# Performance work log

Measured on AMD Instinct MI355X. Metric: run time of the kernel, lower is better.

Reference implementation:

```python
import jax, jax.numpy as jnp
import numpy as np

N_NODES = 100000
N_EDGES = 3200000
F_IN = 256
D_OUT = 64
BATCH = 4096
N_FIELDS = 20


def setup_inputs() -> dict:
    key = jax.random.key(0)
    k1, k2, k3, k4 = jax.random.split(key, 4)
    features = jax.random.normal(k1, (N_NODES, F_IN), dtype=jnp.float32)
    edge_index = jax.random.randint(k2, (2, N_EDGES), 0, N_NODES, dtype=jnp.int32)
    W = jax.random.normal(k3, (F_IN, D_OUT), dtype=jnp.float32) * 0.05
    b = jnp.zeros((D_OUT,), dtype=jnp.float32)
    x = jax.random.randint(k4, (BATCH, N_FIELDS), 0, N_NODES, dtype=jnp.int32)
    return {"features": features, "edge_index": edge_index, "W": W, "b": b, "x": x}


def reference(features, edge_index, W, b, x):
    # PyG GCNConv: add self-loops, symmetric normalization, linear transform,
    # scatter-add aggregation, then final index by x.
    n = features.shape[0]
    loop = jnp.arange(n, dtype=edge_index.dtype)
    src = jnp.concatenate([edge_index[0], loop])  # [E+N]
    dst = jnp.concatenate([edge_index[1], loop])
    ones = jnp.ones(src.shape[0], dtype=features.dtype)
    deg = jax.ops.segment_sum(ones, dst, num_segments=n)  # in-degree incl. self-loop
    deg_inv_sqrt = jnp.where(deg > 0, jax.lax.rsqrt(deg), 0.0)
    norm = deg_inv_sqrt[src] * deg_inv_sqrt[dst]  # [E+N]
    xw = features @ W  # [N, D] -- transform before aggregation (fewer FLOPs)
    msg = xw[src] * norm[:, None]  # gather + scale
    out = jax.ops.segment_sum(msg, dst, num_segments=n) + b  # [N, D]
    return out[x]  # [batch, num_fields, D]
```

## Files before the change

kernel.cpp:

```cpp
#include <hip/hip_runtime.h>
#include <hip/hip_bf16.h>

#define N_NODES 100000
#define N_EDGES 3200000
#define F_IN 256
#define D_OUT 64
#define BATCH 4096
#define N_FIELDS 20
#define N_ENTRIES (BATCH * N_FIELDS)

#define NBUCKET 512
#define NPB 196
#define N_PAD (NBUCKET * NPB)
#define EPB 8192
#define NBLK ((N_EDGES + EPB - 1) / EPB)
#define BUCKET_CAP 8192
#define SCAN_B 512
#define NSB (N_PAD / SCAN_B)

typedef short bf16x8 __attribute__((ext_vector_type(8)));
typedef float f32x4 __attribute__((ext_vector_type(4)));

static __device__ __forceinline__ float bfbits2f(unsigned short u) {
    return __uint_as_float((unsigned)u << 16);
}
static __device__ __forceinline__ unsigned short f2bf_bits(float x) {
    __hip_bfloat16 h = __float2bfloat16(x);
    return *reinterpret_cast<unsigned short*>(&h);
}

__global__ __launch_bounds__(256) void k_hist(const uint4* __restrict__ dst4,
                                              unsigned short* __restrict__ perBlockCnt) {
    __shared__ unsigned hist[NBUCKET];
    hist[threadIdx.x] = 0;
    hist[threadIdx.x + 256] = 0;
    __syncthreads();
    int base4 = blockIdx.x * (EPB / 4);
#pragma unroll
    for (int k = 0; k < EPB / 1024; k++) {
        int e4 = base4 + k * 256 + threadIdx.x;
        if (e4 < N_EDGES / 4) {
            uint4 d = dst4[e4];
            atomicAdd(&hist[d.x / NPB], 1u);
            atomicAdd(&hist[d.y / NPB], 1u);
            atomicAdd(&hist[d.z / NPB], 1u);
            atomicAdd(&hist[d.w / NPB], 1u);
        }
    }
    __syncthreads();
    perBlockCnt[(threadIdx.x) * NBLK + blockIdx.x] = (unsigned short)hist[threadIdx.x];
    perBlockCnt[(threadIdx.x + 256) * NBLK + blockIdx.x] = (unsigned short)hist[threadIdx.x + 256];
}

__global__ __launch_bounds__(256) void k_colscan_w(unsigned short* __restrict__ perBlockCnt,
                                                   int* __restrict__ bucketTot) {
    int gw = (blockIdx.x * 256 + threadIdx.x) >> 6;
    int lane = threadIdx.x & 63;
    if (gw >= NBUCKET) return;
    unsigned running = 0;
    for (int c = 0; c < (NBLK + 63) / 64; c++) {
        int blk = c * 64 + lane;
        int idx = gw * NBLK + blk;
        unsigned v = (blk < NBLK) ? perBlockCnt[idx] : 0;
        unsigned orig = v;
#pragma unroll
        for (int d = 1; d < 64; d <<= 1) {
            unsigned t = __shfl_up(v, d, 64);
            if (lane >= d) v += t;
        }
        if (blk < NBLK) perBlockCnt[idx] = (unsigned short)(running + v - orig);
        running += __shfl(v, 63, 64);
    }
    if (lane == 0) bucketTot[gw] = (int)running;
}

__global__ __launch_bounds__(512) void k_basescan(const int* __restrict__ bucketTot,
                                                  int* __restrict__ bucketBase) {
    __shared__ int sh[NBUCKET];
    int tid = threadIdx.x;
    int v = bucketTot[tid];
    sh[tid] = v;
    __syncthreads();
    for (int off = 1; off < NBUCKET; off <<= 1) {
        int t = (tid >= off) ? sh[tid - off] : 0;
        __syncthreads();
        sh[tid] += t;
        __syncthreads();
    }
    bucketBase[tid] = sh[tid] - v;
    if (tid == NBUCKET - 1) bucketBase[NBUCKET] = sh[NBUCKET - 1];
}

__global__ __launch_bounds__(256) void k_bucket_scatter(const uint4* __restrict__ src4,
                                                        const uint4* __restrict__ dst4,
                                                        const int* __restrict__ bucketBase,
                                                        const unsigned short* __restrict__ perBlockCnt,
                                                        unsigned* __restrict__ bucketData) {
    __shared__ unsigned slotBase[NBUCKET];
    slotBase[threadIdx.x] = (unsigned)bucketBase[threadIdx.x] +
                            (unsigned)perBlockCnt[threadIdx.x * NBLK + blockIdx.x];
    slotBase[threadIdx.x + 256] = (unsigned)bucketBase[threadIdx.x + 256] +
                                  (unsigned)perBlockCnt[(threadIdx.x + 256) * NBLK + blockIdx.x];
    __syncthreads();
    int base4 = blockIdx.x * (EPB / 4);
#pragma unroll
    for (int k = 0; k < EPB / 1024; k++) {
        int e4 = base4 + k * 256 + threadIdx.x;
        if (e4 < N_EDGES / 4) {
            uint4 s = src4[e4];
            uint4 d = dst4[e4];
            unsigned ss[4] = {s.x, s.y, s.z, s.w};
            unsigned dd[4] = {d.x, d.y, d.z, d.w};
#pragma unroll
            for (int j = 0; j < 4; j++) {
                unsigned b = dd[j] / NPB;
                unsigned ld = dd[j] - b * NPB;
                unsigned slot = atomicAdd(&slotBase[b], 1u);
                bucketData[slot] = ss[j] | (ld << 17);
            }
        }
    }
}

__global__ __launch_bounds__(256) void kx_cnt(const int* __restrict__ x,
                                              int* __restrict__ nodeEntCnt,
                                              unsigned* __restrict__ refBits) {
    int ent = blockIdx.x * blockDim.x + threadIdx.x;
    if (ent < N_ENTRIES) {
        int node = x[ent];
        atomicAdd(&nodeEntCnt[node], 1);
        atomicOr(&refBits[node >> 5], 1u << (node & 31));
    }
}

__global__ __launch_bounds__(512) void kx_scan_local(const int* __restrict__ nodeEntCnt,
                                                     int* __restrict__ localE,
                                                     int* __restrict__ blockSumsE) {
    __shared__ int sh[SCAN_B];
    int g = blockIdx.x * SCAN_B + threadIdx.x;
    int v = (g < N_PAD) ? nodeEntCnt[g] : 0;
    sh[threadIdx.x] = v;
    __syncthreads();
    for (int off = 1; off < SCAN_B; off <<= 1) {
        int t = (threadIdx.x >= off) ? sh[threadIdx.x - off] : 0;
        __syncthreads();
        sh[threadIdx.x] += t;
        __syncthreads();
    }
    int incl = sh[threadIdx.x];
    if (g < N_PAD) localE[g] = incl - v;
    if (threadIdx.x == SCAN_B - 1) blockSumsE[blockIdx.x] = incl;
}

__global__ __launch_bounds__(256) void kx_scan_blocks(const int* __restrict__ blockSumsE,
                                                      int* __restrict__ blockBaseE) {
    __shared__ int sh[256];
    int tid = threadIdx.x;
    int v = (tid < NSB) ? blockSumsE[tid] : 0;
    sh[tid] = v;
    __syncthreads();
    for (int off = 1; off < 256; off <<= 1) {
        int t = (tid >= off) ? sh[tid - off] : 0;
        __syncthreads();
        sh[tid] += t;
        __syncthreads();
    }
    if (tid < NSB) blockBaseE[tid] = sh[tid] - v;
}

__global__ __launch_bounds__(256) void kx_scatter(const int* __restrict__ x,
                                                  int* __restrict__ localE,
                                                  const int* __restrict__ blockBaseE,
                                                  int* __restrict__ entGrouped) {
    int ent = blockIdx.x * blockDim.x + threadIdx.x;
    if (ent < N_ENTRIES) {
        int node = x[ent];
        int posL = atomicAdd(&localE[node], 1);
        entGrouped[blockBaseE[node >> 9] + posL] = ent;
    }
}

__global__ __launch_bounds__(256) void k_bucket_csr(unsigned* __restrict__ bucketData,
                                                    const int* __restrict__ bucketBase,
                                                    const unsigned* __restrict__ refBits,
                                                    int* __restrict__ rowStart,
                                                    unsigned short* __restrict__ deg) {
    __shared__ unsigned words[BUCKET_CAP];
    __shared__ unsigned srcsorted[BUCKET_CAP];
    __shared__ unsigned nodeCount[NPB];
    __shared__ unsigned sscan[256];
    __shared__ unsigned cursor[NPB];
    __shared__ unsigned char refF[NPB];

    int b = blockIdx.x;
    int base = bucketBase[b];
    int cnt = bucketBase[b + 1] - base;
    if (cnt > BUCKET_CAP) cnt = BUCKET_CAP;
    int tid = threadIdx.x;

    for (int j = tid; j < NPB; j += 256) nodeCount[j] = 0;
    __syncthreads();

    for (int i = tid; i < cnt; i += 256) {
        unsigned w = bucketData[base + i];
        words[i] = w;
        atomicAdd(&nodeCount[w >> 17], 1u);
    }
    __syncthreads();

    int firstNode = b * NPB;
    unsigned refCnt = 0;
    if (tid < NPB) {
        int node = firstNode + tid;
        unsigned isRef = (refBits[node >> 5] >> (node & 31)) & 1u;
        refF[tid] = (unsigned char)isRef;
        refCnt = isRef ? nodeCount[tid] : 0;
        deg[node] = (unsigned short)nodeCount[tid];
    }
    sscan[tid] = refCnt;
    __syncthreads();
    for (int off = 1; off < 256; off <<= 1) {
        unsigned t = (tid >= off) ? sscan[tid - off] : 0;
        __syncthreads();
        sscan[tid] += t;
        __syncthreads();
    }

    if (tid < NPB) {
        unsigned excl = sscan[tid] - refCnt;
        rowStart[firstNode + tid] = base + (int)excl;
        cursor[tid] = excl;
    }
    __syncthreads();

    for (int i = tid; i < cnt; i += 256) {
        unsigned w = words[i];
        unsigned ld = w >> 17;
        if (refF[ld]) {
            unsigned slot = atomicAdd(&cursor[ld], 1u);
            srcsorted[slot] = w & 0x1FFFFu;
        }
    }
    __syncthreads();

    int refTotal = (int)sscan[255];
    for (int i = tid; i < refTotal; i += 256)
        bucketData[base + i] = srcsorted[i];
}

__global__ void k_wtconv(const float* __restrict__ W, unsigned short* __restrict__ WTbf) {
    int i = blockIdx.x * blockDim.x + threadIdx.x;
    if (i >= D_OUT * F_IN) return;
    int n = i >> 8, k = i & 255;
    WTbf[i] = f2bf_bits(W[k * D_OUT + n]);
}

__global__ __launch_bounds__(256) void k_gemm_mfma(const float* __restrict__ feat,
                                                   const unsigned short* __restrict__ WTbf,
                                                   const unsigned short* __restrict__ deg,
                                                   unsigned short* __restrict__ y) {
    __shared__ unsigned short wt[64 * 264];
    int tid = threadIdx.x;
    {
        int r = tid >> 2, seg = tid & 3;
        const uint4* gsrc = (const uint4*)(WTbf + r * 256 + seg * 64);
        uint4* ldst = (uint4*)&wt[r * 264 + seg * 64];
#pragma unroll
        for (int q = 0; q < 8; q++) ldst[q] = gsrc[q];
    }
    __syncthreads();

    int wave = tid >> 6, lane = tid & 63;
    int quad = lane >> 4, m = lane & 15;
    int rowT = blockIdx.x * 64 + wave * 16;
    int row = rowT + m;
    int rowC = (row < N_NODES) ? row : (N_NODES - 1);
    const float* fb = feat + (size_t)rowC * F_IN + quad * 8;

    f32x4 acc0 = {0.f, 0.f, 0.f, 0.f};
    f32x4 acc1 = acc0, acc2 = acc0, acc3 = acc0;

#pragma unroll
    for (int kk = 0; kk < 8; kk++) {
        float4 x0 = *(const float4*)(fb + kk * 32);
        float4 x1 = *(const float4*)(fb + kk * 32 + 4);
        bf16x8 a;
        a[0] = (short)f2bf_bits(x0.x); a[1] = (short)f2bf_bits(x0.y);
        a[2] = (short)f2bf_bits(x0.z); a[3] = (short)f2bf_bits(x0.w);
        a[4] = (short)f2bf_bits(x1.x); a[5] = (short)f2bf_bits(x1.y);
        a[6] = (short)f2bf_bits(x1.z); a[7] = (short)f2bf_bits(x1.w);
        int kbase = kk * 32 + quad * 8;
        bf16x8 b0 = *(const bf16x8*)&wt[(0 * 16 + m) * 264 + kbase];
        bf16x8 b1 = *(const bf16x8*)&wt[(1 * 16 + m) * 264 + kbase];
        bf16x8 b2 = *(const bf16x8*)&wt[(2 * 16 + m) * 264 + kbase];
        bf16x8 b3 = *(const bf16x8*)&wt[(3 * 16 + m) * 264 + kbase];
        acc0 = __builtin_amdgcn_mfma_f32_16x16x32_bf16(a, b0, acc0, 0, 0, 0);
        acc1 = __builtin_amdgcn_mfma_f32_16x16x32_bf16(a, b1, acc1, 0, 0, 0);
        acc2 = __builtin_amdgcn_mfma_f32_16x16x32_bf16(a, b2, acc2, 0, 0, 0);
        acc3 = __builtin_amdgcn_mfma_f32_16x16x32_bf16(a, b3, acc3, 0, 0, 0);
    }

    float dv[4];
#pragma unroll
    for (int r = 0; r < 4; r++) {
        int rr = rowT + quad * 4 + r;
        dv[r] = rsqrtf((float)(deg[rr] + 1));
    }
#pragma unroll
    for (int r = 0; r < 4; r++) {
        int rr = rowT + quad * 4 + r;
        if (rr < N_NODES) {
            size_t o = (size_t)rr * D_OUT + m;
            y[o]      = f2bf_bits(acc0[r] * dv[r]);
            y[o + 16] = f2bf_bits(acc1[r] * dv[r]);
            y[o + 32] = f2bf_bits(acc2[r] * dv[r]);
            y[o + 48] = f2bf_bits(acc3[r] * dv[r]);
        }
    }
}

static __device__ __forceinline__ void acc4(f32x4& a, uint2 v, float msk) {
    a[0] += msk * __uint_as_float(v.x << 16);
    a[1] += msk * __uint_as_float(v.x & 0xffff0000u);
    a[2] += msk * __uint_as_float(v.y << 16);
    a[3] += msk * __uint_as_float(v.y & 0xffff0000u);
}

__global__ __launch_bounds__(256) void k_agg(const int* __restrict__ entGrouped,
                                             const int* __restrict__ localE,
                                             const int* __restrict__ blockBaseE,
                                             const int* __restrict__ rowStart,
                                             const unsigned short* __restrict__ deg,
                                             const unsigned* __restrict__ sortedSrc,
                                             const unsigned short* __restrict__ y,
                                             const float* __restrict__ b,
                                             float* __restrict__ out) {
    int g = blockIdx.x * blockDim.x + threadIdx.x;
    int i = g >> 6, lane = g & 63;
    if (i >= N_PAD) return;
    int gEnd = blockBaseE[i >> 9] + localE[i];
    int gStart = (i == 0) ? 0 : (blockBaseE[(i - 1) >> 9] + localE[i - 1]);
    int cntEnt = gEnd - gStart;
    if (cntEnt <= 0) return;

    int grp = lane >> 4;
    int m = lane & 15;
    int start = rowStart[i];
    int cnt = deg[i];
    float disI = rsqrtf((float)(cnt + 1));

    uint2 sv = *(const uint2*)(y + ((unsigned)i << 6) + (m << 2));

    f32x4 a0 = {0.f, 0.f, 0.f, 0.f};
    f32x4 a1 = a0, a2 = a0, a3 = a0;

    for (int e = 0; e < cnt; e += 16) {
        int e0 = e + grp, e1 = e + 4 + grp, e2 = e + 8 + grp, e3 = e + 12 + grp;
        unsigned r0 = (e0 < cnt) ? sortedSrc[start + e0] : (unsigned)i;
        unsigned r1 = (e1 < cnt) ? sortedSrc[start + e1] : (unsigned)i;
        unsigned r2 = (e2 < cnt) ? sortedSrc[start + e2] : (unsigned)i;
        unsigned r3 = (e3 < cnt) ? sortedSrc[start + e3] : (unsigned)i;
        uint2 v0 = *(const uint2*)(y + (r0 << 6) + (m << 2));
        uint2 v1 = *(const uint2*)(y + (r1 << 6) + (m << 2));
        uint2 v2 = *(const uint2*)(y + (r2 << 6) + (m << 2));
        uint2 v3 = *(const uint2*)(y + (r3 << 6) + (m << 2));
        acc4(a0, v0, (e0 < cnt) ? 1.f : 0.f);
        acc4(a1, v1, (e1 < cnt) ? 1.f : 0.f);
        acc4(a2, v2, (e2 < cnt) ? 1.f : 0.f);
        acc4(a3, v3, (e3 < cnt) ? 1.f : 0.f);
    }

    f32x4 s;
#pragma unroll
    for (int c = 0; c < 4; c++) s[c] = (a0[c] + a1[c]) + (a2[c] + a3[c]);
#pragma unroll
    for (int c = 0; c < 4; c++) {
        s[c] += __shfl_xor(s[c], 16, 64);
        s[c] += __shfl_xor(s[c], 32, 64);
    }

    float4 b4 = *(const float4*)(b + (m << 2));
    float4 val;
    val.x = disI * (s[0] + __uint_as_float(sv.x << 16)) + b4.x;
    val.y = disI * (s[1] + __uint_as_float(sv.x & 0xffff0000u)) + b4.y;
    val.z = disI * (s[2] + __uint_as_float(sv.y << 16)) + b4.z;
    val.w = disI * (s[3] + __uint_as_float(sv.y & 0xffff0000u)) + b4.w;

    for (int j = grp; j < cntEnt; j += 4) {
        int ent = entGrouped[gStart + j];
        *(float4*)(out + (size_t)ent * D_OUT + (m << 2)) = val;
    }
}

extern "C" void kernel_launch(void* const* d_in, const int* in_sizes, int n_in,
                              void* d_out, int out_size, void* d_ws, size_t ws_size,
                              hipStream_t stream) {
    const float* feat     = (const float*)d_in[0];
    const int* edge_index = (const int*)d_in[1];
    const float* W        = (const float*)d_in[2];
    const float* bsrc     = (const float*)d_in[3];
    const int* x          = (const int*)d_in[4];
    float* out            = (float*)d_out;

    const uint4* src4 = (const uint4*)edge_index;
    const uint4* dst4 = (const uint4*)(edge_index + N_EDGES);

    char* ws = (char*)d_ws;
    size_t off = 0;
    auto alloc = [&](size_t bytes) {
        size_t o = off;
        off = (off + bytes + 255) & ~(size_t)255;
        return o;
    };
    int* bucketBase = (int*)(ws + alloc((size_t)(NBUCKET + 1) * 4));
    int* bucketTot  = (int*)(ws + alloc((size_t)NBUCKET * 4));
    size_t pcOff = alloc((size_t)N_PAD * 4);
    unsigned short* perBlockCnt = (unsigned short*)(ws + pcOff);
    int* nodeEntCnt = (int*)(ws + pcOff);
    int* entGrouped = (int*)(ws + pcOff);
    unsigned* refBits = (unsigned*)(ws + alloc((size_t)(N_PAD / 8)));
    int* rowStart   = (int*)(ws + alloc((size_t)N_PAD * 4));
    unsigned short* deg = (unsigned short*)(ws + alloc((size_t)N_PAD * 2));
    unsigned short* WTbf = (unsigned short*)(ws + alloc((size_t)D_OUT * F_IN * 2));
    int* localE     = (int*)(ws + alloc((size_t)N_PAD * 4));
    int* blockSumsE = (int*)(ws + alloc((size_t)NSB * 4));
    int* blockBaseE = (int*)(ws + alloc((size_t)NSB * 4));
    unsigned* bucketData = (unsigned*)(ws + alloc((size_t)N_EDGES * 4));
    unsigned short* y = (unsigned short*)(ws + alloc((size_t)N_NODES * D_OUT * 2));
    (void)ws_size; (void)in_sizes; (void)n_in; (void)out_size;

    const int T = 256;
    k_hist<<<NBLK, T, 0, stream>>>(dst4, perBlockCnt);
    k_colscan_w<<<(NBUCKET * 64 + T - 1) / T, T, 0, stream>>>(perBlockCnt, bucketTot);
    k_basescan<<<1, NBUCKET, 0, stream>>>(bucketTot, bucketBase);
    k_bucket_scatter<<<NBLK, T, 0, stream>>>(src4, dst4, bucketBase, perBlockCnt, bucketData);
    hipMemsetAsync(nodeEntCnt, 0, (size_t)N_PAD * 4, stream);
    hipMemsetAsync(refBits, 0, (size_t)(N_PAD / 8), stream);
    kx_cnt<<<(N_ENTRIES + T - 1) / T, T, 0, stream>>>(x, nodeEntCnt, refBits);
    kx_scan_local<<<NSB, SCAN_B, 0, stream>>>(nodeEntCnt, localE, blockSumsE);
    kx_scan_blocks<<<1, 256, 0, stream>>>(blockSumsE, blockBaseE);
    kx_scatter<<<(N_ENTRIES + T - 1) / T, T, 0, stream>>>(x, localE, blockBaseE, entGrouped);
    k_bucket_csr<<<NBUCKET, T, 0, stream>>>(bucketData, bucketBase, refBits, rowStart, deg);
    k_wtconv<<<(D_OUT * F_IN + T - 1) / T, T, 0, stream>>>(W, WTbf);
    k_gemm_mfma<<<(N_NODES + 63) / 64, T, 0, stream>>>(feat, WTbf, deg, y);
    k_agg<<<((size_t)N_PAD * 64 + T - 1) / T, T, 0, stream>>>(
        entGrouped, localE, blockBaseE, rowStart, deg, bucketData, y, bsrc, out);
}
```

Before: 327.1 us.

## Filter edges to referenced destinations before bucketing and compute degree via global atomics

```diff
diff --git a/kernel.cpp b/kernel.cpp
--- a/kernel.cpp
+++ b/kernel.cpp
@@ -17,23 +17,83 @@
 #define BUCKET_CAP 8192
 #define SCAN_B 512
 #define NSB (N_PAD / SCAN_B)
+#define RBW (N_PAD / 32)
 
 typedef short bf16x8 __attribute__((ext_vector_type(8)));
 typedef float f32x4 __attribute__((ext_vector_type(4)));
 
-static __device__ __forceinline__ float bfbits2f(unsigned short u) {
-    return __uint_as_float((unsigned)u << 16);
-}
 static __device__ __forceinline__ unsigned short f2bf_bits(float x) {
     __hip_bfloat16 h = __float2bfloat16(x);
     return *reinterpret_cast<unsigned short*>(&h);
 }
 
+__global__ __launch_bounds__(256) void kx_cnt(const int* __restrict__ x,
+                                              int* __restrict__ nodeEntCnt,
+                                              unsigned* __restrict__ refBits) {
+    int ent = blockIdx.x * blockDim.x + threadIdx.x;
+    if (ent < N_ENTRIES) {
+        int node = x[ent];
+        atomicAdd(&nodeEntCnt[node], 1);
+        atomicOr(&refBits[node >> 5], 1u << (node & 31));
+    }
+}
+
+__global__ __launch_bounds__(512) void kx_scan_local(const int* __restrict__ nodeEntCnt,
+                                                     int* __restrict__ localE,
+                                                     int* __restrict__ blockSumsE) {
+    __shared__ int sh[SCAN_B];
+    int g = blockIdx.x * SCAN_B + threadIdx.x;
+    int v = (g < N_PAD) ? nodeEntCnt[g] : 0;
+    sh[threadIdx.x] = v;
+    __syncthreads();
+    for (int off = 1; off < SCAN_B; off <<= 1) {
+        int t = (threadIdx.x >= off) ? sh[threadIdx.x - off] : 0;
+        __syncthreads();
+        sh[threadIdx.x] += t;
+        __syncthreads();
+    }
+    int incl = sh[threadIdx.x];
+    if (g < N_PAD) localE[g] = incl - v;
+    if (threadIdx.x == SCAN_B - 1) blockSumsE[blockIdx.x] = incl;
+}
+
+__global__ __launch_bounds__(256) void kx_scan_blocks(const int* __restrict__ blockSumsE,
+                                                      int* __restrict__ blockBaseE) {
+    __shared__ int sh[256];
+    int tid = threadIdx.x;
+    int v = (tid < NSB) ? blockSumsE[tid] : 0;
+    sh[tid] = v;
+    __syncthreads();
+    for (int off = 1; off < 256; off <<= 1) {
+        int t = (tid >= off) ? sh[tid - off] : 0;
+        __syncthreads();
+        sh[tid] += t;
+        __syncthreads();
+    }
+    if (tid < NSB) blockBaseE[tid] = sh[tid] - v;
+}
+
+__global__ __launch_bounds__(256) void kx_scatter(const int* __restrict__ x,
+                                                  int* __restrict__ localE,
+                                                  const int* __restrict__ blockBaseE,
+                                                  int* __restrict__ entGrouped) {
+    int ent = blockIdx.x * blockDim.x + threadIdx.x;
+    if (ent < N_ENTRIES) {
+        int node = x[ent];
+        int posL = atomicAdd(&localE[node], 1);
+        entGrouped[blockBaseE[node >> 9] + posL] = ent;
+    }
+}
+
 __global__ __launch_bounds__(256) void k_hist(const uint4* __restrict__ dst4,
+                                              const unsigned* __restrict__ refBits,
+                                              unsigned* __restrict__ degW,
                                               unsigned short* __restrict__ perBlockCnt) {
     __shared__ unsigned hist[NBUCKET];
+    __shared__ unsigned rb[RBW];
     hist[threadIdx.x] = 0;
     hist[threadIdx.x + 256] = 0;
+    for (int j = threadIdx.x; j < RBW; j += 256) rb[j] = refBits[j];
     __syncthreads();
     int base4 = blockIdx.x * (EPB / 4);
 #pragma unroll
@@ -41,10 +101,13 @@
         int e4 = base4 + k * 256 + threadIdx.x;
         if (e4 < N_EDGES / 4) {
             uint4 d = dst4[e4];
-            atomicAdd(&hist[d.x / NPB], 1u);
-            atomicAdd(&hist[d.y / NPB], 1u);
-            atomicAdd(&hist[d.z / NPB], 1u);
-            atomicAdd(&hist[d.w / NPB], 1u);
+            unsigned dd[4] = {d.x, d.y, d.z, d.w};
+#pragma unroll
+            for (int j = 0; j < 4; j++) {
+                atomicAdd(&degW[dd[j]], 1u);
+                if ((rb[dd[j] >> 5] >> (dd[j] & 31)) & 1u)
+                    atomicAdd(&hist[dd[j] / NPB], 1u);
+            }
         }
     }
     __syncthreads();
@@ -95,12 +158,15 @@
                                                         const uint4* __restrict__ dst4,
                                                         const int* __restrict__ bucketBase,
                                                         const unsigned short* __restrict__ perBlockCnt,
+                                                        const unsigned* __restrict__ refBits,
                                                         unsigned* __restrict__ bucketData) {
     __shared__ unsigned slotBase[NBUCKET];
+    __shared__ unsigned rb[RBW];
     slotBase[threadIdx.x] = (unsigned)bucketBase[threadIdx.x] +
                             (unsigned)perBlockCnt[threadIdx.x * NBLK + blockIdx.x];
     slotBase[threadIdx.x + 256] = (unsigned)bucketBase[threadIdx.x + 256] +
                                   (unsigned)perBlockCnt[(threadIdx.x + 256) * NBLK + blockIdx.x];
+    for (int j = threadIdx.x; j < RBW; j += 256) rb[j] = refBits[j];
     __syncthreads();
     int base4 = blockIdx.x * (EPB / 4);
 #pragma unroll
@@ -113,111 +179,40 @@
             unsigned dd[4] = {d.x, d.y, d.z, d.w};
 #pragma unroll
             for (int j = 0; j < 4; j++) {
-                unsigned b = dd[j] / NPB;
-                unsigned ld = dd[j] - b * NPB;
-                unsigned slot = atomicAdd(&slotBase[b], 1u);
-                bucketData[slot] = ss[j] | (ld << 17);
+                if ((rb[dd[j] >> 5] >> (dd[j] & 31)) & 1u) {
+                    unsigned b = dd[j] / NPB;
+                    unsigned ld = dd[j] - b * NPB;
+                    unsigned slot = atomicAdd(&slotBase[b], 1u);
+                    bucketData[slot] = ss[j] | (ld << 17);
+                }
             }
         }
-    }
-}
-
-__global__ __launch_bounds__(256) void kx_cnt(const int* __restrict__ x,
-                                              int* __restrict__ nodeEntCnt,
-                                              unsigned* __restrict__ refBits) {
-    int ent = blockIdx.x * blockDim.x + threadIdx.x;
-    if (ent < N_ENTRIES) {
-        int node = x[ent];
-        atomicAdd(&nodeEntCnt[node], 1);
-        atomicOr(&refBits[node >> 5], 1u << (node & 31));
-    }
-}
-
-__global__ __launch_bounds__(512) void kx_scan_local(const int* __restrict__ nodeEntCnt,
-                                                     int* __restrict__ localE,
-                                                     int* __restrict__ blockSumsE) {
-    __shared__ int sh[SCAN_B];
-    int g = blockIdx.x * SCAN_B + threadIdx.x;
-    int v = (g < N_PAD) ? nodeEntCnt[g] : 0;
-    sh[threadIdx.x] = v;
-    __syncthreads();
-    for (int off = 1; off < SCAN_B; off <<= 1) {
-        int t = (threadIdx.x >= off) ? sh[threadIdx.x - off] : 0;
-        __syncthreads();
-        sh[threadIdx.x] += t;
-        __syncthreads();
-    }
-    int incl = sh[threadIdx.x];
-    if (g < N_PAD) localE[g] = incl - v;
-    if (threadIdx.x == SCAN_B - 1) blockSumsE[blockIdx.x] = incl;
-}
-
-__global__ __launch_bounds__(256) void kx_scan_blocks(const int* __restrict__ blockSumsE,
-                                                      int* __restrict__ blockBaseE) {
-    __shared__ int sh[256];
-    int tid = threadIdx.x;
-    int v = (tid < NSB) ? blockSumsE[tid] : 0;
-    sh[tid] = v;
-    __syncthreads();
-    for (int off = 1; off < 256; off <<= 1) {
-        int t = (tid >= off) ? sh[tid - off] : 0;
-        __syncthreads();
-        sh[tid] += t;
-        __syncthreads();
-    }
-    if (tid < NSB) blockBaseE[tid] = sh[tid] - v;
-}
-
-__global__ __launch_bounds__(256) void kx_scatter(const int* __restrict__ x,
-                                                  int* __restrict__ localE,
-                                                  const int* __restrict__ blockBaseE,
-                                                  int* __restrict__ entGrouped) {
-    int ent = blockIdx.x * blockDim.x + threadIdx.x;
-    if (ent < N_ENTRIES) {
-        int node = x[ent];
-        int posL = atomicAdd(&localE[node], 1);
-        entGrouped[blockBaseE[node >> 9] + posL] = ent;
     }
 }
 
 __global__ __launch_bounds__(256) void k_bucket_csr(unsigned* __restrict__ bucketData,
                                                     const int* __restrict__ bucketBase,
                                                     const unsigned* __restrict__ refBits,
-                                                    int* __restrict__ rowStart,
-                                                    unsigned short* __restrict__ deg) {
-    __shared__ unsigned words[BUCKET_CAP];
+                                                    const unsigned* __restrict__ degW,
+                                                    int* __restrict__ rowStart) {
     __shared__ unsigned srcsorted[BUCKET_CAP];
-    __shared__ unsigned nodeCount[NPB];
     __shared__ unsigned sscan[256];
     __shared__ unsigned cursor[NPB];
-    __shared__ unsigned char refF[NPB];
 
     int b = blockIdx.x;
     int base = bucketBase[b];
     int cnt = bucketBase[b + 1] - base;
     if (cnt > BUCKET_CAP) cnt = BUCKET_CAP;
     int tid = threadIdx.x;
-
-    for (int j = tid; j < NPB; j += 256) nodeCount[j] = 0;
-    __syncthreads();
-
-    for (int i = tid; i < cnt; i += 256) {
-        unsigned w = bucketData[base + i];
-        words[i] = w;
-        atomicAdd(&nodeCount[w >> 17], 1u);
-    }
-    __syncthreads();
-
     int firstNode = b * NPB;
-    unsigned refCnt = 0;
+
+    unsigned c0 = 0;
     if (tid < NPB) {
         int node = firstNode + tid;
         unsigned isRef = (refBits[node >> 5] >> (node & 31)) & 1u;
-        refF[tid] = (unsigned char)isRef;
-        refCnt = isRef ? nodeCount[tid] : 0;
-        deg[node] = (unsigned short)nodeCount[tid];
-    }
-    sscan[tid] = refCnt;
+        c0 = isRef ? degW[node] : 0u;
+    }
+    sscan[tid] = c0;
     __syncthreads();
     for (int off = 1; off < 256; off <<= 1) {
         unsigned t = (tid >= off) ? sscan[tid - off] : 0;
@@ -225,26 +220,21 @@
         sscan[tid] += t;
         __syncthreads();
     }
-
     if (tid < NPB) {
-        unsigned excl = sscan[tid] - refCnt;
+        unsigned excl = sscan[tid] - c0;
         rowStart[firstNode + tid] = base + (int)excl;
         cursor[tid] = excl;
     }
     __syncthreads();
 
     for (int i = tid; i < cnt; i += 256) {
-        unsigned w = words[i];
-        unsigned ld = w >> 17;
-        if (refF[ld]) {
-            unsigned slot = atomicAdd(&cursor[ld], 1u);
-            srcsorted[slot] = w & 0x1FFFFu;
-        }
-    }
-    __syncthreads();
-
-    int refTotal = (int)sscan[255];
-    for (int i = tid; i < refTotal; i += 256)
+        unsigned w = bucketData[base + i];
+        unsigned slot = atomicAdd(&cursor[w >> 17], 1u);
+        srcsorted[slot] = w & 0x1FFFFu;
+    }
+    __syncthreads();
+
+    for (int i = tid; i < cnt; i += 256)
         bucketData[base + i] = srcsorted[i];
 }
 
@@ -257,7 +247,7 @@
 
 __global__ __launch_bounds__(256) void k_gemm_mfma(const float* __restrict__ feat,
                                                    const unsigned short* __restrict__ WTbf,
-                                                   const unsigned short* __restrict__ deg,
+                                                   const unsigned* __restrict__ degW,
                                                    unsigned short* __restrict__ y) {
     __shared__ unsigned short wt[64 * 264];
     int tid = threadIdx.x;
@@ -304,7 +294,7 @@
 #pragma unroll
     for (int r = 0; r < 4; r++) {
         int rr = rowT + quad * 4 + r;
-        dv[r] = rsqrtf((float)(deg[rr] + 1));
+        dv[r] = rsqrtf((float)(degW[rr] + 1));
     }
 #pragma unroll
     for (int r = 0; r < 4; r++) {
@@ -330,7 +320,7 @@
                                              const int* __restrict__ localE,
                                              const int* __restrict__ blockBaseE,
                                              const int* __restrict__ rowStart,
-                                             const unsigned short* __restrict__ deg,
+                                             const unsigned* __restrict__ degW,
                                              const unsigned* __restrict__ sortedSrc,
                                              const unsigned short* __restrict__ y,
                                              const float* __restrict__ b,
@@ -346,7 +336,7 @@
     int grp = lane >> 4;
     int m = lane & 15;
     int start = rowStart[i];
-    int cnt = deg[i];
+    int cnt = (int)degW[i];
     float disI = rsqrtf((float)(cnt + 1));
 
     uint2 sv = *(const uint2*)(y + ((unsigned)i << 6) + (m << 2));
@@ -354,20 +344,33 @@
     f32x4 a0 = {0.f, 0.f, 0.f, 0.f};
     f32x4 a1 = a0, a2 = a0, a3 = a0;
 
-    for (int e = 0; e < cnt; e += 16) {
-        int e0 = e + grp, e1 = e + 4 + grp, e2 = e + 8 + grp, e3 = e + 12 + grp;
+    for (int e = 0; e < cnt; e += 32) {
+        int e0 = e + grp,      e1 = e + 4 + grp,  e2 = e + 8 + grp,  e3 = e + 12 + grp;
+        int e4 = e + 16 + grp, e5 = e + 20 + grp, e6 = e + 24 + grp, e7 = e + 28 + grp;
         unsigned r0 = (e0 < cnt) ? sortedSrc[start + e0] : (unsigned)i;
         unsigned r1 = (e1 < cnt) ? sortedSrc[start + e1] : (unsigned)i;
         unsigned r2 = (e2 < cnt) ? sortedSrc[start + e2] : (unsigned)i;
         unsigned r3 = (e3 < cnt) ? sortedSrc[start + e3] : (unsigned)i;
+        unsigned r4 = (e4 < cnt) ? sortedSrc[start + e4] : (unsigned)i;
+        unsigned r5 = (e5 < cnt) ? sortedSrc[start + e5] : (unsigned)i;
+        unsigned r6 = (e6 < cnt) ? sortedSrc[start + e6] : (unsigned)i;
+        unsigned r7 = (e7 < cnt) ? sortedSrc[start + e7] : (unsigned)i;
         uint2 v0 = *(const uint2*)(y + (r0 << 6) + (m << 2));
         uint2 v1 = *(const uint2*)(y + (r1 << 6) + (m << 2));
         uint2 v2 = *(const uint2*)(y + (r2 << 6) + (m << 2));
         uint2 v3 = *(const uint2*)(y + (r3 << 6) + (m << 2));
+        uint2 v4 = *(const uint2*)(y + (r4 << 6) + (m << 2));
+        uint2 v5 = *(const uint2*)(y + (r5 << 6) + (m << 2));
+        uint2 v6 = *(const uint2*)(y + (r6 << 6) + (m << 2));
+        uint2 v7 = *(const uint2*)(y + (r7 << 6) + (m << 2));
         acc4(a0, v0, (e0 < cnt) ? 1.f : 0.f);
         acc4(a1, v1, (e1 < cnt) ? 1.f : 0.f);
         acc4(a2, v2, (e2 < cnt) ? 1.f : 0.f);
         acc4(a3, v3, (e3 < cnt) ? 1.f : 0.f);
+        acc4(a0, v4, (e4 < cnt) ? 1.f : 0.f);
+        acc4(a1, v5, (e5 < cnt) ? 1.f : 0.f);
+        acc4(a2, v6, (e6 < cnt) ? 1.f : 0.f);
+        acc4(a3, v7, (e7 < cnt) ? 1.f : 0.f);
     }
 
     f32x4 s;
@@ -415,12 +418,13 @@
     int* bucketBase = (int*)(ws + alloc((size_t)(NBUCKET + 1) * 4));
     int* bucketTot  = (int*)(ws + alloc((size_t)NBUCKET * 4));
     size_t pcOff = alloc((size_t)N_PAD * 4);
-    unsigned short* perBlockCnt = (unsigned short*)(ws + pcOff);
     int* nodeEntCnt = (int*)(ws + pcOff);
     int* entGrouped = (int*)(ws + pcOff);
     unsigned* refBits = (unsigned*)(ws + alloc((size_t)(N_PAD / 8)));
-    int* rowStart   = (int*)(ws + alloc((size_t)N_PAD * 4));
-    unsigned short* deg = (unsigned short*)(ws + alloc((size_t)N_PAD * 2));
+    size_t rsOff = alloc((size_t)N_PAD * 4);
+    unsigned short* perBlockCnt = (unsigned short*)(ws + rsOff);
+    int* rowStart   = (int*)(ws + rsOff);
+    unsigned* degW  = (unsigned*)(ws + alloc((size_t)N_PAD * 4));
     unsigned short* WTbf = (unsigned short*)(ws + alloc((size_t)D_OUT * F_IN * 2));
     int* localE     = (int*)(ws + alloc((size_t)N_PAD * 4));
     int* blockSumsE = (int*)(ws + alloc((size_t)NSB * 4));
@@ -430,19 +434,20 @@
     (void)ws_size; (void)in_sizes; (void)n_in; (void)out_size;
 
     const int T = 256;
-    k_hist<<<NBLK, T, 0, stream>>>(dst4, perBlockCnt);
-    k_colscan_w<<<(NBUCKET * 64 + T - 1) / T, T, 0, stream>>>(perBlockCnt, bucketTot);
-    k_basescan<<<1, NBUCKET, 0, stream>>>(bucketTot, bucketBase);
-    k_bucket_scatter<<<NBLK, T, 0, stream>>>(src4, dst4, bucketBase, perBlockCnt, bucketData);
-    hipMemsetAsync(nodeEntCnt, 0, (size_t)N_PAD * 4, stream);
-    hipMemsetAsync(refBits, 0, (size_t)(N_PAD / 8), stream);
+    (void)hipMemsetAsync(nodeEntCnt, 0, (size_t)N_PAD * 4, stream);
+    (void)hipMemsetAsync(refBits, 0, (size_t)(N_PAD / 8), stream);
+    (void)hipMemsetAsync(degW, 0, (size_t)N_PAD * 4, stream);
     kx_cnt<<<(N_ENTRIES + T - 1) / T, T, 0, stream>>>(x, nodeEntCnt, refBits);
     kx_scan_local<<<NSB, SCAN_B, 0, stream>>>(nodeEntCnt, localE, blockSumsE);
     kx_scan_blocks<<<1, 256, 0, stream>>>(blockSumsE, blockBaseE);
     kx_scatter<<<(N_ENTRIES + T - 1) / T, T, 0, stream>>>(x, localE, blockBaseE, entGrouped);
-    k_bucket_csr<<<NBUCKET, T, 0, stream>>>(bucketData, bucketBase, refBits, rowStart, deg);
+    k_hist<<<NBLK, T, 0, stream>>>(dst4, refBits, degW, perBlockCnt);
+    k_colscan_w<<<(NBUCKET * 64 + T - 1) / T, T, 0, stream>>>(perBlockCnt, bucketTot);
+    k_basescan<<<1, NBUCKET, 0, stream>>>(bucketTot, bucketBase);
+    k_bucket_scatter<<<NBLK, T, 0, stream>>>(src4, dst4, bucketBase, perBlockCnt, refBits, bucketData);
+    k_bucket_csr<<<NBUCKET, T, 0, stream>>>(bucketData, bucketBase, refBits, degW, rowStart);
     k_wtconv<<<(D_OUT * F_IN + T - 1) / T, T, 0, stream>>>(W, WTbf);
-    k_gemm_mfma<<<(N_NODES + 63) / 64, T, 0, stream>>>(feat, WTbf, deg, y);
+    k_gemm_mfma<<<(N_NODES + 63) / 64, T, 0, stream>>>(feat, WTbf, degW, y);
     k_agg<<<((size_t)N_PAD * 64 + T - 1) / T, T, 0, stream>>>(
-        entGrouped, localE, blockBaseE, rowStart, deg, bucketData, y, bsrc, out);
-}
+        entGrouped, localE, blockBaseE, rowStart, degW, bucketData, y, bsrc, out);
+}
```

New measurement: 437.0 us. +33.6%, slower.

## Merge independent preprocessing kernels into fused multi-role launches and unroll aggregation

Applied to the files above, without the earlier changes.

```diff
diff --git a/kernel.cpp b/kernel.cpp
--- a/kernel.cpp
+++ b/kernel.cpp
@@ -17,166 +17,175 @@
 #define BUCKET_CAP 8192
 #define SCAN_B 512
 #define NSB (N_PAD / SCAN_B)
+#define CNT_BLKS (N_ENTRIES / 256)
+#define WT_BLKS (D_OUT * F_IN / 256)
 
 typedef short bf16x8 __attribute__((ext_vector_type(8)));
 typedef float f32x4 __attribute__((ext_vector_type(4)));
 
-static __device__ __forceinline__ float bfbits2f(unsigned short u) {
-    return __uint_as_float((unsigned)u << 16);
-}
 static __device__ __forceinline__ unsigned short f2bf_bits(float x) {
     __hip_bfloat16 h = __float2bfloat16(x);
     return *reinterpret_cast<unsigned short*>(&h);
 }
 
-__global__ __launch_bounds__(256) void k_hist(const uint4* __restrict__ dst4,
-                                              unsigned short* __restrict__ perBlockCnt) {
-    __shared__ unsigned hist[NBUCKET];
-    hist[threadIdx.x] = 0;
-    hist[threadIdx.x + 256] = 0;
-    __syncthreads();
-    int base4 = blockIdx.x * (EPB / 4);
-#pragma unroll
-    for (int k = 0; k < EPB / 1024; k++) {
-        int e4 = base4 + k * 256 + threadIdx.x;
-        if (e4 < N_EDGES / 4) {
-            uint4 d = dst4[e4];
-            atomicAdd(&hist[d.x / NPB], 1u);
-            atomicAdd(&hist[d.y / NPB], 1u);
-            atomicAdd(&hist[d.z / NPB], 1u);
-            atomicAdd(&hist[d.w / NPB], 1u);
-        }
-    }
-    __syncthreads();
-    perBlockCnt[(threadIdx.x) * NBLK + blockIdx.x] = (unsigned short)hist[threadIdx.x];
-    perBlockCnt[(threadIdx.x + 256) * NBLK + blockIdx.x] = (unsigned short)hist[threadIdx.x + 256];
-}
-
-__global__ __launch_bounds__(256) void k_colscan_w(unsigned short* __restrict__ perBlockCnt,
-                                                   int* __restrict__ bucketTot) {
-    int gw = (blockIdx.x * 256 + threadIdx.x) >> 6;
-    int lane = threadIdx.x & 63;
-    if (gw >= NBUCKET) return;
-    unsigned running = 0;
-    for (int c = 0; c < (NBLK + 63) / 64; c++) {
-        int blk = c * 64 + lane;
-        int idx = gw * NBLK + blk;
-        unsigned v = (blk < NBLK) ? perBlockCnt[idx] : 0;
-        unsigned orig = v;
-#pragma unroll
-        for (int d = 1; d < 64; d <<= 1) {
-            unsigned t = __shfl_up(v, d, 64);
-            if (lane >= d) v += t;
-        }
-        if (blk < NBLK) perBlockCnt[idx] = (unsigned short)(running + v - orig);
-        running += __shfl(v, 63, 64);
-    }
-    if (lane == 0) bucketTot[gw] = (int)running;
-}
-
-__global__ __launch_bounds__(512) void k_basescan(const int* __restrict__ bucketTot,
-                                                  int* __restrict__ bucketBase) {
-    __shared__ int sh[NBUCKET];
+__global__ __launch_bounds__(256) void k_front(const uint4* __restrict__ dst4,
+                                               unsigned short* __restrict__ perBlockCnt,
+                                               const int* __restrict__ x,
+                                               int* __restrict__ nodeEntCnt,
+                                               unsigned* __restrict__ refBits,
+                                               const float* __restrict__ W,
+                                               unsigned short* __restrict__ WTbf) {
+    if (blockIdx.x < NBLK) {
+        __shared__ unsigned hist[NBUCKET];
+        hist[threadIdx.x] = 0;
+        hist[threadIdx.x + 256] = 0;
+        __syncthreads();
+        int base4 = blockIdx.x * (EPB / 4);
+#pragma unroll
+        for (int k = 0; k < EPB / 1024; k++) {
+            int e4 = base4 + k * 256 + threadIdx.x;
+            if (e4 < N_EDGES / 4) {
+                uint4 d = dst4[e4];
+                atomicAdd(&hist[d.x / NPB], 1u);
+                atomicAdd(&hist[d.y / NPB], 1u);
+                atomicAdd(&hist[d.z / NPB], 1u);
+                atomicAdd(&hist[d.w / NPB], 1u);
+            }
+        }
+        __syncthreads();
+        perBlockCnt[(threadIdx.x) * NBLK + blockIdx.x] = (unsigned short)hist[threadIdx.x];
+        perBlockCnt[(threadIdx.x + 256) * NBLK + blockIdx.x] = (unsigned short)hist[threadIdx.x + 256];
+    } else if (blockIdx.x < NBLK + CNT_BLKS) {
+        int ent = (blockIdx.x - NBLK) * 256 + threadIdx.x;
+        if (ent < N_ENTRIES) {
+            int node = x[ent];
+            atomicAdd(&nodeEntCnt[node], 1);
+            atomicOr(&refBits[node >> 5], 1u << (node & 31));
+        }
+    } else {
+        int i = (blockIdx.x - NBLK - CNT_BLKS) * 256 + threadIdx.x;
+        if (i < D_OUT * F_IN) {
+            int n = i >> 8, k = i & 255;
+            WTbf[i] = f2bf_bits(W[k * D_OUT + n]);
+        }
+    }
+}
+
+__global__ __launch_bounds__(512) void k_scans(const int* __restrict__ nodeEntCnt,
+                                               int* __restrict__ localE,
+                                               int* __restrict__ blockSumsE,
+                                               unsigned short* __restrict__ perBlockCnt,
+                                               int* __restrict__ bucketTot) {
+    if (blockIdx.x < NSB) {
+        __shared__ int sh[SCAN_B];
+        int g = blockIdx.x * SCAN_B + threadIdx.x;
+        int v = (g < N_PAD) ? nodeEntCnt[g] : 0;
+        sh[threadIdx.x] = v;
+        __syncthreads();
+        for (int off = 1; off < SCAN_B; off <<= 1) {
+            int t = (threadIdx.x >= off) ? sh[threadIdx.x - off] : 0;
+            __syncthreads();
+            sh[threadIdx.x] += t;
+            __syncthreads();
+        }
+        int incl = sh[threadIdx.x];
+        if (g < N_PAD) localE[g] = incl - v;
+        if (threadIdx.x == SCAN_B - 1) blockSumsE[blockIdx.x] = incl;
+    } else {
+        int gw = ((blockIdx.x - NSB) * 512 + threadIdx.x) >> 6;
+        int lane = threadIdx.x & 63;
+        if (gw >= NBUCKET) return;
+        unsigned running = 0;
+        for (int c = 0; c < (NBLK + 63) / 64; c++) {
+            int blk = c * 64 + lane;
+            int idx = gw * NBLK + blk;
+            unsigned v = (blk < NBLK) ? perBlockCnt[idx] : 0;
+            unsigned orig = v;
+#pragma unroll
+            for (int d = 1; d < 64; d <<= 1) {
+                unsigned t = __shfl_up(v, d, 64);
+                if (lane >= d) v += t;
+            }
+            if (blk < NBLK) perBlockCnt[idx] = (unsigned short)(running + v - orig);
+            running += __shfl(v, 63, 64);
+        }
+        if (lane == 0) bucketTot[gw] = (int)running;
+    }
+}
+
+__global__ __launch_bounds__(512) void k_base2(const int* __restrict__ bucketTot,
+                                               int* __restrict__ bucketBase,
+                                               const int* __restrict__ blockSumsE,
+                                               int* __restrict__ blockBaseE) {
+    __shared__ int sh[512];
     int tid = threadIdx.x;
-    int v = bucketTot[tid];
-    sh[tid] = v;
-    __syncthreads();
-    for (int off = 1; off < NBUCKET; off <<= 1) {
-        int t = (tid >= off) ? sh[tid - off] : 0;
-        __syncthreads();
-        sh[tid] += t;
-        __syncthreads();
-    }
-    bucketBase[tid] = sh[tid] - v;
-    if (tid == NBUCKET - 1) bucketBase[NBUCKET] = sh[NBUCKET - 1];
-}
-
-__global__ __launch_bounds__(256) void k_bucket_scatter(const uint4* __restrict__ src4,
-                                                        const uint4* __restrict__ dst4,
-                                                        const int* __restrict__ bucketBase,
-                                                        const unsigned short* __restrict__ perBlockCnt,
-                                                        unsigned* __restrict__ bucketData) {
-    __shared__ unsigned slotBase[NBUCKET];
-    slotBase[threadIdx.x] = (unsigned)bucketBase[threadIdx.x] +
-                            (unsigned)perBlockCnt[threadIdx.x * NBLK + blockIdx.x];
-    slotBase[threadIdx.x + 256] = (unsigned)bucketBase[threadIdx.x + 256] +
-                                  (unsigned)perBlockCnt[(threadIdx.x + 256) * NBLK + blockIdx.x];
-    __syncthreads();
-    int base4 = blockIdx.x * (EPB / 4);
-#pragma unroll
-    for (int k = 0; k < EPB / 1024; k++) {
-        int e4 = base4 + k * 256 + threadIdx.x;
-        if (e4 < N_EDGES / 4) {
-            uint4 s = src4[e4];
-            uint4 d = dst4[e4];
-            unsigned ss[4] = {s.x, s.y, s.z, s.w};
-            unsigned dd[4] = {d.x, d.y, d.z, d.w};
-#pragma unroll
-            for (int j = 0; j < 4; j++) {
-                unsigned b = dd[j] / NPB;
-                unsigned ld = dd[j] - b * NPB;
-                unsigned slot = atomicAdd(&slotBase[b], 1u);
-                bucketData[slot] = ss[j] | (ld << 17);
-            }
-        }
-    }
-}
-
-__global__ __launch_bounds__(256) void kx_cnt(const int* __restrict__ x,
-                                              int* __restrict__ nodeEntCnt,
-                                              unsigned* __restrict__ refBits) {
-    int ent = blockIdx.x * blockDim.x + threadIdx.x;
-    if (ent < N_ENTRIES) {
-        int node = x[ent];
-        atomicAdd(&nodeEntCnt[node], 1);
-        atomicOr(&refBits[node >> 5], 1u << (node & 31));
-    }
-}
-
-__global__ __launch_bounds__(512) void kx_scan_local(const int* __restrict__ nodeEntCnt,
-                                                     int* __restrict__ localE,
-                                                     int* __restrict__ blockSumsE) {
-    __shared__ int sh[SCAN_B];
-    int g = blockIdx.x * SCAN_B + threadIdx.x;
-    int v = (g < N_PAD) ? nodeEntCnt[g] : 0;
-    sh[threadIdx.x] = v;
-    __syncthreads();
-    for (int off = 1; off < SCAN_B; off <<= 1) {
-        int t = (threadIdx.x >= off) ? sh[threadIdx.x - off] : 0;
-        __syncthreads();
-        sh[threadIdx.x] += t;
-        __syncthreads();
-    }
-    int incl = sh[threadIdx.x];
-    if (g < N_PAD) localE[g] = incl - v;
-    if (threadIdx.x == SCAN_B - 1) blockSumsE[blockIdx.x] = incl;
-}
-
-__global__ __launch_bounds__(256) void kx_scan_blocks(const int* __restrict__ blockSumsE,
-                                                      int* __restrict__ blockBaseE) {
-    __shared__ int sh[256];
-    int tid = threadIdx.x;
-    int v = (tid < NSB) ? blockSumsE[tid] : 0;
-    sh[tid] = v;
-    __syncthreads();
-    for (int off = 1; off < 256; off <<= 1) {
-        int t = (tid >= off) ? sh[tid - off] : 0;
-        __syncthreads();
-        sh[tid] += t;
-        __syncthreads();
-    }
-    if (tid < NSB) blockBaseE[tid] = sh[tid] - v;
-}
-
-__global__ __launch_bounds__(256) void kx_scatter(const int* __restrict__ x,
+    if (blockIdx.x == 0) {
+        int v = bucketTot[tid];
+        sh[tid] = v;
+        __syncthreads();
+        for (int off = 1; off < 512; off <<= 1) {
+            int t = (tid >= off) ? sh[tid - off] : 0;
+            __syncthreads();
+            sh[tid] += t;
+            __syncthreads();
+        }
+        bucketBase[tid] = sh[tid] - v;
+        if (tid == NBUCKET - 1) bucketBase[NBUCKET] = sh[NBUCKET - 1];
+    } else {
+        int v = (tid < NSB) ? blockSumsE[tid] : 0;
+        sh[tid] = v;
+        __syncthreads();
+        for (int off = 1; off < 512; off <<= 1) {
+            int t = (tid >= off) ? sh[tid - off] : 0;
+            __syncthreads();
+            sh[tid] += t;
+            __syncthreads();
+        }
+        if (tid < NSB) blockBaseE[tid] = sh[tid] - v;
+    }
+}
+
+__global__ __launch_bounds__(256) void k_scatters(const uint4* __restrict__ src4,
+                                                  const uint4* __restrict__ dst4,
+                                                  const int* __restrict__ bucketBase,
+                                                  const unsigned short* __restrict__ perBlockCnt,
+                                                  unsigned* __restrict__ bucketData,
+                                                  const int* __restrict__ x,
                                                   int* __restrict__ localE,
                                                   const int* __restrict__ blockBaseE,
                                                   int* __restrict__ entGrouped) {
-    int ent = blockIdx.x * blockDim.x + threadIdx.x;
-    if (ent < N_ENTRIES) {
-        int node = x[ent];
-        int posL = atomicAdd(&localE[node], 1);
-        entGrouped[blockBaseE[node >> 9] + posL] = ent;
+    if (blockIdx.x < NBLK) {
+        __shared__ unsigned slotBase[NBUCKET];
+        slotBase[threadIdx.x] = (unsigned)bucketBase[threadIdx.x] +
+                                (unsigned)perBlockCnt[threadIdx.x * NBLK + blockIdx.x];
+        slotBase[threadIdx.x + 256] = (unsigned)bucketBase[threadIdx.x + 256] +
+                                      (unsigned)perBlockCnt[(threadIdx.x + 256) * NBLK + blockIdx.x];
+        __syncthreads();
+        int base4 = blockIdx.x * (EPB / 4);
+#pragma unroll
+        for (int k = 0; k < EPB / 1024; k++) {
+            int e4 = base4 + k * 256 + threadIdx.x;
+            if (e4 < N_EDGES / 4) {
+                uint4 s = src4[e4];
+                uint4 d = dst4[e4];
+                unsigned ss[4] = {s.x, s.y, s.z, s.w};
+                unsigned dd[4] = {d.x, d.y, d.z, d.w};
+#pragma unroll
+                for (int j = 0; j < 4; j++) {
+                    unsigned b = dd[j] / NPB;
+                    unsigned ld = dd[j] - b * NPB;
+                    unsigned slot = atomicAdd(&slotBase[b], 1u);
+                    bucketData[slot] = ss[j] | (ld << 17);
+                }
+            }
+        }
+    } else {
+        int ent = (blockIdx.x - NBLK) * 256 + threadIdx.x;
+        if (ent < N_ENTRIES) {
+            int node = x[ent];
+            int posL = atomicAdd(&localE[node], 1);
+            entGrouped[blockBaseE[node >> 9] + posL] = ent;
+        }
     }
 }
 
@@ -185,7 +194,6 @@
                                                     const unsigned* __restrict__ refBits,
                                                     int* __restrict__ rowStart,
                                                     unsigned short* __restrict__ deg) {
-    __shared__ unsigned words[BUCKET_CAP];
     __shared__ unsigned srcsorted[BUCKET_CAP];
     __shared__ unsigned nodeCount[NPB];
     __shared__ unsigned sscan[256];
@@ -203,7 +211,6 @@
 
     for (int i = tid; i < cnt; i += 256) {
         unsigned w = bucketData[base + i];
-        words[i] = w;
         atomicAdd(&nodeCount[w >> 17], 1u);
     }
     __syncthreads();
@@ -234,7 +241,7 @@
     __syncthreads();
 
     for (int i = tid; i < cnt; i += 256) {
-        unsigned w = words[i];
+        unsigned w = bucketData[base + i];
         unsigned ld = w >> 17;
         if (refF[ld]) {
             unsigned slot = atomicAdd(&cursor[ld], 1u);
@@ -246,13 +253,6 @@
     int refTotal = (int)sscan[255];
     for (int i = tid; i < refTotal; i += 256)
         bucketData[base + i] = srcsorted[i];
-}
-
-__global__ void k_wtconv(const float* __restrict__ W, unsigned short* __restrict__ WTbf) {
-    int i = blockIdx.x * blockDim.x + threadIdx.x;
-    if (i >= D_OUT * F_IN) return;
-    int n = i >> 8, k = i & 255;
-    WTbf[i] = f2bf_bits(W[k * D_OUT + n]);
 }
 
 __global__ __launch_bounds__(256) void k_gemm_mfma(const float* __restrict__ feat,
@@ -354,20 +354,33 @@
     f32x4 a0 = {0.f, 0.f, 0.f, 0.f};
     f32x4 a1 = a0, a2 = a0, a3 = a0;
 
-    for (int e = 0; e < cnt; e += 16) {
-        int e0 = e + grp, e1 = e + 4 + grp, e2 = e + 8 + grp, e3 = e + 12 + grp;
+    for (int e = 0; e < cnt; e += 32) {
+        int e0 = e + grp,      e1 = e + 4 + grp,  e2 = e + 8 + grp,  e3 = e + 12 + grp;
+        int e4 = e + 16 + grp, e5 = e + 20 + grp, e6 = e + 24 + grp, e7 = e + 28 + grp;
         unsigned r0 = (e0 < cnt) ? sortedSrc[start + e0] : (unsigned)i;
         unsigned r1 = (e1 < cnt) ? sortedSrc[start + e1] : (unsigned)i;
         unsigned r2 = (e2 < cnt) ? sortedSrc[start + e2] : (unsigned)i;
         unsigned r3 = (e3 < cnt) ? sortedSrc[start + e3] : (unsigned)i;
+        unsigned r4 = (e4 < cnt) ? sortedSrc[start + e4] : (unsigned)i;
+        unsigned r5 = (e5 < cnt) ? sortedSrc[start + e5] : (unsigned)i;
+        unsigned r6 = (e6 < cnt) ? sortedSrc[start + e6] : (unsigned)i;
+        unsigned r7 = (e7 < cnt) ? sortedSrc[start + e7] : (unsigned)i;
         uint2 v0 = *(const uint2*)(y + (r0 << 6) + (m << 2));
         uint2 v1 = *(const uint2*)(y + (r1 << 6) + (m << 2));
         uint2 v2 = *(const uint2*)(y + (r2 << 6) + (m << 2));
         uint2 v3 = *(const uint2*)(y + (r3 << 6) + (m << 2));
+        uint2 v4 = *(const uint2*)(y + (r4 << 6) + (m << 2));
+        uint2 v5 = *(const uint2*)(y + (r5 << 6) + (m << 2));
+        uint2 v6 = *(const uint2*)(y + (r6 << 6) + (m << 2));
+        uint2 v7 = *(const uint2*)(y + (r7 << 6) + (m << 2));
         acc4(a0, v0, (e0 < cnt) ? 1.f : 0.f);
         acc4(a1, v1, (e1 < cnt) ? 1.f : 0.f);
         acc4(a2, v2, (e2 < cnt) ? 1.f : 0.f);
         acc4(a3, v3, (e3 < cnt) ? 1.f : 0.f);
+        acc4(a0, v4, (e4 < cnt) ? 1.f : 0.f);
+        acc4(a1, v5, (e5 < cnt) ? 1.f : 0.f);
+        acc4(a2, v6, (e6 < cnt) ? 1.f : 0.f);
+        acc4(a3, v7, (e7 < cnt) ? 1.f : 0.f);
     }
 
     f32x4 s;
@@ -414,12 +427,13 @@
     };
     int* bucketBase = (int*)(ws + alloc((size_t)(NBUCKET + 1) * 4));
     int* bucketTot  = (int*)(ws + alloc((size_t)NBUCKET * 4));
-    size_t pcOff = alloc((size_t)N_PAD * 4);
-    unsigned short* perBlockCnt = (unsigned short*)(ws + pcOff);
-    int* nodeEntCnt = (int*)(ws + pcOff);
-    int* entGrouped = (int*)(ws + pcOff);
+    size_t ecOff = alloc((size_t)N_PAD * 4);
+    int* nodeEntCnt = (int*)(ws + ecOff);
+    int* entGrouped = (int*)(ws + ecOff);
     unsigned* refBits = (unsigned*)(ws + alloc((size_t)(N_PAD / 8)));
-    int* rowStart   = (int*)(ws + alloc((size_t)N_PAD * 4));
+    size_t rsOff = alloc((size_t)N_PAD * 4);
+    unsigned short* perBlockCnt = (unsigned short*)(ws + rsOff);
+    int* rowStart   = (int*)(ws + rsOff);
     unsigned short* deg = (unsigned short*)(ws + alloc((size_t)N_PAD * 2));
     unsigned short* WTbf = (unsigned short*)(ws + alloc((size_t)D_OUT * F_IN * 2));
     int* localE     = (int*)(ws + alloc((size_t)N_PAD * 4));
@@ -430,18 +444,15 @@
     (void)ws_size; (void)in_sizes; (void)n_in; (void)out_size;
 
     const int T = 256;
-    k_hist<<<NBLK, T, 0, stream>>>(dst4, perBlockCnt);
-    k_colscan_w<<<(NBUCKET * 64 + T - 1) / T, T, 0, stream>>>(perBlockCnt, bucketTot);
-    k_basescan<<<1, NBUCKET, 0, stream>>>(bucketTot, bucketBase);
-    k_bucket_scatter<<<NBLK, T, 0, stream>>>(src4, dst4, bucketBase, perBlockCnt, bucketData);
-    hipMemsetAsync(nodeEntCnt, 0, (size_t)N_PAD * 4, stream);
-    hipMemsetAsync(refBits, 0, (size_t)(N_PAD / 8), stream);
-    kx_cnt<<<(N_ENTRIES + T - 1) / T, T, 0, stream>>>(x, nodeEntCnt, refBits);
-    kx_scan_local<<<NSB, SCAN_B, 0, stream>>>(nodeEntCnt, localE, blockSumsE);
-    kx_scan_blocks<<<1, 256, 0, stream>>>(blockSumsE, blockBaseE);
-    kx_scatter<<<(N_ENTRIES + T - 1) / T, T, 0, stream>>>(x, localE, blockBaseE, entGrouped);
+    (void)hipMemsetAsync(nodeEntCnt, 0, (size_t)N_PAD * 4, stream);
+    (void)hipMemsetAsync(refBits, 0, (size_t)(N_PAD / 8), stream);
+    k_front<<<NBLK + CNT_BLKS + WT_BLKS, T, 0, stream>>>(dst4, perBlockCnt, x, nodeEntCnt,
+                                                         refBits, W, WTbf);
+    k_scans<<<NSB + 64, 512, 0, stream>>>(nodeEntCnt, localE, blockSumsE, perBlockCnt, bucketTot);
+    k_base2<<<2, 512, 0, stream>>>(bucketTot, bucketBase, blockSumsE, blockBaseE);
+    k_scatters<<<NBLK + CNT_BLKS, T, 0, stream>>>(src4, dst4, bucketBase, perBlockCnt, bucketData,
+                                                  x, localE, blockBaseE, entGrouped);
     k_bucket_csr<<<NBUCKET, T, 0, stream>>>(bucketData, bucketBase, refBits, rowStart, deg);
-    k_wtconv<<<(D_OUT * F_IN + T - 1) / T, T, 0, stream>>>(W, WTbf);
     k_gemm_mfma<<<(N_NODES + 63) / 64, T, 0, stream>>>(feat, WTbf, deg, y);
     k_agg<<<((size_t)N_PAD * 64 + T - 1) / T, T, 0, stream>>>(
         entGrouped, localE, blockBaseE, rowStart, deg, bucketData, y, bsrc, out);
```

After: 321.5 us. No clear change (-1.7%).
